# Kernel optimization log

Measured on AMD Instinct MI355X. Metric: run time of the kernel, lower is better.

Reference implementation:

```python
import jax, jax.numpy as jnp
import numpy as np

D_MODEL = 1024
N_HEADS = 16
HEAD_DIM = D_MODEL // N_HEADS  # 64


def setup_inputs() -> dict:
    key = jax.random.key(0)
    k1, k2, k3 = jax.random.split(key, 3)
    B, T = 2, 2048
    x = jax.random.normal(k1, (B, T, D_MODEL), dtype=jnp.float32)
    # nn.Linear(d, 3d) weight applied as x @ W (stored transposed vs torch)
    W_qkv = jax.random.normal(k2, (D_MODEL, 3 * D_MODEL), dtype=jnp.float32) / np.sqrt(D_MODEL)
    W_proj = jax.random.normal(k3, (D_MODEL, D_MODEL), dtype=jnp.float32) / np.sqrt(D_MODEL)
    return {"x": x, "W_qkv": W_qkv, "W_proj": W_proj}


def reference(x, W_qkv, W_proj):
    B, T, D = x.shape
    qkv = x @ W_qkv  # [B, T, 3D]
    qkv = qkv.reshape(B, T, 3, N_HEADS, HEAD_DIM)
    qkv = jnp.transpose(qkv, (2, 0, 3, 1, 4))  # [3, B, H, T, hd]
    q, k, v = qkv[0], qkv[1], qkv[2]
    # muP 'readout' attn_score: scale by 1/head_dim (instead of 1/sqrt(head_dim))
    attn = jnp.einsum('bhqd,bhkd->bhqk', q, k) / HEAD_DIM  # [B, H, T, T]
    attn = jax.nn.softmax(attn, axis=-1)
    out = jnp.einsum('bhqk,bhkd->bhqd', attn, v)  # [B, H, T, hd]
    out = jnp.transpose(out, (0, 2, 1, 3)).reshape(B, T, D)
    return out @ W_proj
```

## Files before the change

### kernel.cpp

```cpp
#include <hip/hip_runtime.h>
#include <hip/hip_bf16.h>
#include <hip/hip_fp16.h>
#include <stdint.h>

#define B_    2
#define T_    2048
#define DM    1024
#define NH    16
#define HD    64
#define M_    (B_ * T_)
#define N_QKV (3 * DM)

typedef __attribute__((ext_vector_type(8))) __bf16 bf16x8;
typedef __attribute__((ext_vector_type(4))) float  v4f;
typedef __attribute__((ext_vector_type(2))) __fp16 fp16x2;
typedef __attribute__((ext_vector_type(4))) _Float16 h4;
typedef __attribute__((ext_vector_type(8))) _Float16 h8;
typedef __hip_bfloat16 bf16;

#define EXP_SC 0.022542110013890053f

__device__ __forceinline__ void gld_lds16(const void* g, void* l) {
  __builtin_amdgcn_global_load_lds(
      (const __attribute__((address_space(1))) void*)(g),
      (__attribute__((address_space(3))) void*)(l), 16, 0, 0);
}


__global__ __launch_bounds__(256) void prep(
    const float* __restrict__ x, const float* __restrict__ Wqkv,
    const float* __restrict__ Wproj, bf16* __restrict__ Xb,
    bf16* __restrict__ WqkvT, bf16* __restrict__ WprojT) {
  const int f = blockIdx.x;
  if (f < 4096) {
    int i = (f * 256 + threadIdx.x) * 4;
    float4 v = *(const float4*)(x + i);
    union { bf16 h[4]; ushort4 u; } r;
    r.h[0] = __float2bfloat16(v.x); r.h[1] = __float2bfloat16(v.y);
    r.h[2] = __float2bfloat16(v.z); r.h[3] = __float2bfloat16(v.w);
    *(ushort4*)(Xb + i) = r.u;
    return;
  }
  __shared__ float tile[32][33];
  const float* in; bf16* out; int C, bx, by;
  if (f < 4096 + 3072) { int g = f - 4096; bx = g % 96; by = g / 96;
                         in = Wqkv;  out = WqkvT;  C = N_QKV; }
  else                 { int g = f - 7168; bx = g % 32; by = g / 32;
                         in = Wproj; out = WprojT; C = DM; }
  const int R = DM;
  int tx = threadIdx.x & 31, ty = threadIdx.x >> 5;
  int c0 = bx * 32, r0 = by * 32;
  #pragma unroll
  for (int i = ty; i < 32; i += 8)
    tile[i][tx] = in[(size_t)(r0 + i) * C + c0 + tx];
  __syncthreads();
  #pragma unroll
  for (int i = ty; i < 32; i += 8)
    out[(size_t)(c0 + i) * R + r0 + tx] = __float2bfloat16(tile[tx][i]);
}

__global__ __launch_bounds__(256) void transpose_v(
    const _Float16* __restrict__ in, _Float16* __restrict__ out) {
  __shared__ _Float16 tl[64][72];
  const int tid = threadIdx.x, bh = blockIdx.y, t0 = blockIdx.x * 64;
  const size_t ib = (size_t)bh * T_ * HD, ob = (size_t)bh * HD * T_;
  #pragma unroll
  for (int i = 0; i < 2; ++i) {
    int flat = (i * 256 + tid) * 8;
    int r = flat >> 6, c = flat & 63;
    *(uint4*)(&tl[r][c]) = *(const uint4*)(in + ib + (size_t)(t0 + r) * HD + c);
  }
  __syncthreads();
  int d = tid >> 2, c0 = (tid & 3) * 16;
  #pragma unroll
  for (int j = 0; j < 16; j += 8) {
    union { _Float16 h[8]; uint4 u; } pk;
    #pragma unroll
    for (int k2 = 0; k2 < 8; ++k2) pk.h[k2] = tl[c0 + j + k2][d];
    *(uint4*)(out + ob + (size_t)d * T_ + t0 + c0 + j) = pk.u;
  }
}

template <int MODE>
__global__ __launch_bounds__(256) void gemm_bt(
    const bf16* __restrict__ A, const bf16* __restrict__ BT,
    float* __restrict__ Cf, bf16* __restrict__ qb, bf16* __restrict__ kb,
    _Float16* __restrict__ vb, int M, int N, int K) {
  __shared__ bf16 As[128 * 64];
  __shared__ bf16 Bs[128 * 64];
  const int tid = threadIdx.x;
  const int l = tid & 63, w = tid >> 6;
  const int wm = w >> 1, wn = w & 1;
  const int m0 = blockIdx.y * 128, n0 = blockIdx.x * 128;
  const int fr = l & 15;
  const int lg = l >> 4;

  v4f acc[4][4] = {};

  for (int kt = 0; kt < K; kt += 64) {
    __syncthreads();
    #pragma unroll
    for (int i = 0; i < 4; ++i) {
      int p = i * 256 + tid;
      int row = p >> 3, g = (p & 7) ^ (row & 7);
      gld_lds16(A + (size_t)(m0 + row) * K + kt + g * 8, As + p * 8);
      gld_lds16(BT + (size_t)(n0 + row) * K + kt + g * 8, Bs + p * 8);
    }
    __syncthreads();
    #pragma unroll
    for (int kk = 0; kk < 64; kk += 32) {
      const int gl = (kk >> 3) + lg;
      bf16x8 af[4], bfr[4];
      #pragma unroll
      for (int i = 0; i < 4; ++i) {
        int row = wm * 64 + i * 16 + fr;
        af[i] = *(const bf16x8*)(As + row * 64 + (gl ^ (fr & 7)) * 8);
      }
      #pragma unroll
      for (int i = 0; i < 4; ++i) {
        int row = wn * 64 + i * 16 + fr;
        bfr[i] = *(const bf16x8*)(Bs + row * 64 + (gl ^ (fr & 7)) * 8);
      }
      #pragma unroll
      for (int mi = 0; mi < 4; ++mi)
        #pragma unroll
        for (int ni = 0; ni < 4; ++ni)
          acc[mi][ni] = __builtin_amdgcn_mfma_f32_16x16x32_bf16(
              af[mi], bfr[ni], acc[mi][ni], 0, 0, 0);
    }
  }

  #pragma unroll
  for (int mi = 0; mi < 4; ++mi) {
    #pragma unroll
    for (int ni = 0; ni < 4; ++ni) {
      #pragma unroll
      for (int r = 0; r < 4; ++r) {
        int gm = m0 + wm * 64 + mi * 16 + (l >> 4) * 4 + r;
        int gn = n0 + wn * 64 + ni * 16 + (l & 15);
        float v = acc[mi][ni][r];
        if constexpr (MODE == 0) {
          Cf[(size_t)gm * N + gn] = v;
        } else {
          int b = gm >> 11, t = gm & 2047;
          int s = gn >> 10, h = (gn >> 6) & 15, d = gn & 63;
          size_t bh = (size_t)(b * NH + h);
          if (s == 0)      qb[(bh * T_ + t) * HD + d] = __float2bfloat16(v * EXP_SC);
          else if (s == 1) kb[(bh * T_ + t) * HD + d] = __float2bfloat16(v);
          else             vb[(bh * T_ + t) * HD + d] = (_Float16)v;
        }
      }
    }
  }
}

__global__ __launch_bounds__(256) void gemm_bt_n64(
    const bf16* __restrict__ A, const bf16* __restrict__ BT,
    float* __restrict__ Cf, int M, int N, int K) {
  __shared__ bf16 As[128 * 64];
  __shared__ bf16 Bs[64 * 64];
  const int tid = threadIdx.x;
  const int l = tid & 63, w = tid >> 6;
  const int wm = w >> 1, wn = w & 1;
  const int m0 = blockIdx.y * 128, n0 = blockIdx.x * 64;
  const int fr = l & 15;
  const int lg = l >> 4;

  v4f acc[4][2] = {};

  for (int kt = 0; kt < K; kt += 64) {
    __syncthreads();
    #pragma unroll
    for (int i = 0; i < 4; ++i) {
      int p = i * 256 + tid;
      int row = p >> 3, g = (p & 7) ^ (row & 7);
      gld_lds16(A + (size_t)(m0 + row) * K + kt + g * 8, As + p * 8);
    }
    #pragma unroll
    for (int i = 0; i < 2; ++i) {
      int p = i * 256 + tid;
      int row = p >> 3, g = (p & 7) ^ (row & 7);
      gld_lds16(BT + (size_t)(n0 + row) * K + kt + g * 8, Bs + p * 8);
    }
    __syncthreads();
    #pragma unroll
    for (int kk = 0; kk < 64; kk += 32) {
      const int gl = (kk >> 3) + lg;
      bf16x8 af[4], bfr[2];
      #pragma unroll
      for (int i = 0; i < 4; ++i) {
        int row = wm * 64 + i * 16 + fr;
        af[i] = *(const bf16x8*)(As + row * 64 + (gl ^ (fr & 7)) * 8);
      }
      #pragma unroll
      for (int i = 0; i < 2; ++i) {
        int row = wn * 32 + i * 16 + fr;
        bfr[i] = *(const bf16x8*)(Bs + row * 64 + (gl ^ (fr & 7)) * 8);
      }
      #pragma unroll
      for (int mi = 0; mi < 4; ++mi)
        #pragma unroll
        for (int ni = 0; ni < 2; ++ni)
          acc[mi][ni] = __builtin_amdgcn_mfma_f32_16x16x32_bf16(
              af[mi], bfr[ni], acc[mi][ni], 0, 0, 0);
    }
  }

  #pragma unroll
  for (int mi = 0; mi < 4; ++mi)
    #pragma unroll
    for (int ni = 0; ni < 2; ++ni)
      #pragma unroll
      for (int r = 0; r < 4; ++r) {
        int gm = m0 + wm * 64 + mi * 16 + (l >> 4) * 4 + r;
        int gn = n0 + wn * 32 + ni * 16 + (l & 15);
        Cf[(size_t)gm * N + gn] = acc[mi][ni][r];
      }
}

__global__ __launch_bounds__(256) void flash_attn(
    const bf16* __restrict__ Qg, const bf16* __restrict__ Kg,
    const _Float16* __restrict__ VTg, bf16* __restrict__ Og) {
  __shared__ char smem[53248];
  bf16*     Ks = (bf16*)smem;
  _Float16* Vs = (_Float16*)(smem + 16384);
  _Float16 (*Ps)[40] = (_Float16(*)[40])(smem + 32768);
  float*    Obuf = (float*)smem;
  float*    Lbuf = (float*)(smem + 34816);

  const int tid = threadIdx.x, l = tid & 63, w = tid >> 6;
  const int qh = w & 1, kh = w >> 1;
  const int fr = l & 15, fk = (l >> 4) * 8, g4 = (l >> 4) * 4, lg = l >> 4;
  const int bh = blockIdx.y, qt = blockIdx.x;
  const int q0 = qt * 128 + qh * 64;
  const size_t base  = (size_t)bh * T_ * HD;
  const size_t baseV = (size_t)bh * HD * T_;
  _Float16 (*Pw)[40] = Ps + w * 64;

  bf16x8 qB[4][2];
  #pragma unroll
  for (int qf = 0; qf < 4; ++qf)
    #pragma unroll
    for (int kki = 0; kki < 2; ++kki)
      qB[qf][kki] = *(const bf16x8*)(
          Qg + base + (size_t)(q0 + qf * 16 + fr) * HD + kki * 32 + fk);

  h8 ones;
  #pragma unroll
  for (int j = 0; j < 8; ++j) ones[j] = (_Float16)1.0f;

  v4f o[4][4] = {};
  v4f lacc[4] = {};

  for (int kt = 0; kt < T_; kt += 128) {
    __syncthreads();
    #pragma unroll
    for (int i = 0; i < 4; ++i) {
      int p = i * 256 + tid;
      int krow = p >> 3, kg = (p & 7) ^ (krow & 7);
      gld_lds16(Kg + base + (size_t)(kt + krow) * HD + kg * 8, Ks + p * 8);
      int vrow = p >> 4, vg = (p & 15) ^ (vrow & 15);
      gld_lds16(VTg + baseV + (size_t)vrow * T_ + kt + vg * 8, Vs + p * 8);
    }
    __syncthreads();

    #pragma unroll
    for (int c = 0; c < 2; ++c) {
      const int kkg = kh * 2 + c;
      #pragma unroll
      for (int hf = 0; hf < 2; ++hf) {
        const int kf = kkg * 2 + hf;
        v4f st[4] = {};
        #pragma unroll
        for (int kki = 0; kki < 2; ++kki) {
          int row = kf * 16 + fr;
          bf16x8 ak = *(const bf16x8*)(
              Ks + row * 64 + ((kki * 4 + lg) ^ (fr & 7)) * 8);
          #pragma unroll
          for (int qf = 0; qf < 4; ++qf)
            st[qf] = __builtin_amdgcn_mfma_f32_16x16x32_bf16(
                ak, qB[qf][kki], st[qf], 0, 0, 0);
        }
        #pragma unroll
        for (int qf = 0; qf < 4; ++qf) {
          union { fp16x2 p2[2]; h4 p4; } u;
          u.p2[0] = __builtin_amdgcn_cvt_pkrtz(
              __builtin_amdgcn_exp2f(st[qf][0]),
              __builtin_amdgcn_exp2f(st[qf][1]));
          u.p2[1] = __builtin_amdgcn_cvt_pkrtz(
              __builtin_amdgcn_exp2f(st[qf][2]),
              __builtin_amdgcn_exp2f(st[qf][3]));
          *(h4*)(&Pw[qf * 16 + fr][hf * 16 + g4]) = u.p4;
        }
      }
      h8 ap[4], bv[4];
      #pragma unroll
      for (int qf = 0; qf < 4; ++qf)
        ap[qf] = *(const h8*)(&Pw[qf * 16 + fr][fk]);
      #pragma unroll
      for (int nf = 0; nf < 4; ++nf) {
        int row = nf * 16 + fr;
        bv[nf] = *(const h8*)(Vs + row * 128 + ((kkg * 4 + lg) ^ fr) * 8);
      }
      #pragma unroll
      for (int qf = 0; qf < 4; ++qf) {
        lacc[qf] = __builtin_amdgcn_mfma_f32_16x16x32_f16(
            ap[qf], ones, lacc[qf], 0, 0, 0);
        #pragma unroll
        for (int nf = 0; nf < 4; ++nf)
          o[qf][nf] = __builtin_amdgcn_mfma_f32_16x16x32_f16(
              ap[qf], bv[nf], o[qf][nf], 0, 0, 0);
      }
    }
  }

  __syncthreads();
  if (w >= 2) {
    #pragma unroll
    for (int qf = 0; qf < 4; ++qf)
      #pragma unroll
      for (int r = 0; r < 4; ++r) {
        int row = qf * 16 + g4 + r;
        #pragma unroll
        for (int nf = 0; nf < 4; ++nf)
          Obuf[(qh * 64 + row) * 68 + nf * 16 + fr] = o[qf][nf][r];
        if (fr == 0) Lbuf[qh * 64 + row] = lacc[qf][r];
      }
  }
  __syncthreads();
  if (w < 2) {
    int b = bh >> 4, h = bh & 15;
    #pragma unroll
    for (int qf = 0; qf < 4; ++qf) {
      #pragma unroll
      for (int r = 0; r < 4; ++r) {
        int row = qf * 16 + g4 + r;
        float inv = 1.f / (lacc[qf][r] + Lbuf[qh * 64 + row]);
        int t = q0 + row;
        #pragma unroll
        for (int nf = 0; nf < 4; ++nf) {
          float val = o[qf][nf][r] + Obuf[(qh * 64 + row) * 68 + nf * 16 + fr];
          Og[((size_t)(b * T_ + t)) * DM + h * HD + nf * 16 + fr] =
              __float2bfloat16(val * inv);
        }
      }
    }
  }
}

extern "C" void kernel_launch(void* const* d_in, const int* in_sizes, int n_in,
                              void* d_out, int out_size, void* d_ws, size_t ws_size,
                              hipStream_t stream) {
  const float* x     = (const float*)d_in[0];
  const float* Wqkv  = (const float*)d_in[1];
  const float* Wproj = (const float*)d_in[2];
  float* out = (float*)d_out;
  char* ws = (char*)d_ws;

  bf16*     Xb     = (bf16*)(ws);
  bf16*     WqkvT  = (bf16*)(ws + (size_t)( 8u << 20));
  bf16*     WprojT = (bf16*)(ws + (size_t)(14u << 20));
  bf16*     Qb     = (bf16*)(ws + (size_t)(16u << 20));
  bf16*     Kb     = (bf16*)(ws + (size_t)(24u << 20));
  _Float16* VTh    = (_Float16*)(ws + (size_t)(32u << 20));
  _Float16* Vh     = (_Float16*)(ws + (size_t)(40u << 20));
  bf16*     Ab     = (bf16*)(ws + (size_t)(40u << 20));

  prep<<<8192, 256, 0, stream>>>(x, Wqkv, Wproj, Xb, WqkvT, WprojT);

  gemm_bt<1><<<dim3(N_QKV / 128, M_ / 128), 256, 0, stream>>>(
      Xb, WqkvT, nullptr, Qb, Kb, Vh, M_, N_QKV, DM);

  transpose_v<<<dim3(T_ / 64, B_ * NH), 256, 0, stream>>>(Vh, VTh);

  flash_attn<<<dim3(T_ / 128, B_ * NH), 256, 0, stream>>>(Qb, Kb, VTh, Ab);

  gemm_bt_n64<<<dim3(DM / 64, M_ / 128), 256, 0, stream>>>(
      Ab, WprojT, out, M_, DM, DM);
}
```

Baseline: 188.4 us.

## Fuse V transpose into QKV GEMM epilogue and split attention keys across blocks

The QKV GEMM now writes V already transposed, staging it through shared memory in its epilogue, so the separate transpose kernel is gone. Flash attention is split into two key halves via grid z to double the block count. Each half atomically adds its unnormalized output and row sums into fp32 buffers, and a new normalize kernel converts them to bf16. This adds two memsets, atomics traffic and an extra pass over a 16MB fp32 buffer in exchange for more parallelism. Summation order of the atomics is nondeterministic.

New measurement: 258.4 us. +37.2%, slower.

```diff
diff --git a/kernel.cpp b/kernel.cpp
--- a/kernel.cpp
+++ b/kernel.cpp
@@ -59,41 +59,21 @@
     out[(size_t)(c0 + i) * R + r0 + tx] = __float2bfloat16(tile[tx][i]);
 }
 
-__global__ __launch_bounds__(256) void transpose_v(
-    const _Float16* __restrict__ in, _Float16* __restrict__ out) {
-  __shared__ _Float16 tl[64][72];
-  const int tid = threadIdx.x, bh = blockIdx.y, t0 = blockIdx.x * 64;
-  const size_t ib = (size_t)bh * T_ * HD, ob = (size_t)bh * HD * T_;
-  #pragma unroll
-  for (int i = 0; i < 2; ++i) {
-    int flat = (i * 256 + tid) * 8;
-    int r = flat >> 6, c = flat & 63;
-    *(uint4*)(&tl[r][c]) = *(const uint4*)(in + ib + (size_t)(t0 + r) * HD + c);
-  }
-  __syncthreads();
-  int d = tid >> 2, c0 = (tid & 3) * 16;
-  #pragma unroll
-  for (int j = 0; j < 16; j += 8) {
-    union { _Float16 h[8]; uint4 u; } pk;
-    #pragma unroll
-    for (int k2 = 0; k2 < 8; ++k2) pk.h[k2] = tl[c0 + j + k2][d];
-    *(uint4*)(out + ob + (size_t)d * T_ + t0 + c0 + j) = pk.u;
-  }
-}
-
 template <int MODE>
 __global__ __launch_bounds__(256) void gemm_bt(
     const bf16* __restrict__ A, const bf16* __restrict__ BT,
     float* __restrict__ Cf, bf16* __restrict__ qb, bf16* __restrict__ kb,
-    _Float16* __restrict__ vb, int M, int N, int K) {
-  __shared__ bf16 As[128 * 64];
-  __shared__ bf16 Bs[128 * 64];
+    _Float16* __restrict__ vtb, int M, int N, int K) {
+  __shared__ char smem[35840];
+  bf16* As = (bf16*)smem;
+  bf16* Bs = (bf16*)(smem + 16384);
   const int tid = threadIdx.x;
   const int l = tid & 63, w = tid >> 6;
   const int wm = w >> 1, wn = w & 1;
   const int m0 = blockIdx.y * 128, n0 = blockIdx.x * 128;
   const int fr = l & 15;
   const int lg = l >> 4;
+  const int g4 = lg * 4;
 
   v4f acc[4][4] = {};
 
@@ -130,14 +110,49 @@
     }
   }
 
+  if constexpr (MODE == 1) {
+    if (n0 >= 2048) {
+      const int b = m0 >> 11;
+      const int vt0 = m0 & 2047;
+      const int hbase = ((n0 - 2048) >> 6) & 15;
+      _Float16 (*Vt)[136] = (_Float16(*)[136])smem;
+      #pragma unroll
+      for (int half = 0; half < 2; ++half) {
+        __syncthreads();
+        if (wn == half) {
+          #pragma unroll
+          for (int mi = 0; mi < 4; ++mi) {
+            int trow = wm * 64 + mi * 16 + g4;
+            #pragma unroll
+            for (int ni = 0; ni < 4; ++ni) {
+              h4 pv;
+              #pragma unroll
+              for (int r = 0; r < 4; ++r) pv[r] = (_Float16)acc[mi][ni][r];
+              *(h4*)(&Vt[ni * 16 + fr][trow]) = pv;
+            }
+          }
+        }
+        __syncthreads();
+        size_t bh = (size_t)(b * NH + ((hbase + half) & 15));
+        #pragma unroll
+        for (int i = 0; i < 4; ++i) {
+          int p = i * 256 + tid;
+          int d = p >> 4, tg = (p & 15) * 8;
+          *(uint4*)(vtb + (bh * HD + d) * T_ + vt0 + tg) = *(uint4*)(&Vt[d][tg]);
+        }
+      }
+      return;
+    }
+  }
+
   #pragma unroll
   for (int mi = 0; mi < 4; ++mi) {
     #pragma unroll
     for (int ni = 0; ni < 4; ++ni) {
       #pragma unroll
       for (int r = 0; r < 4; ++r) {
-        int gm = m0 + wm * 64 + mi * 16 + (l >> 4) * 4 + r;
-        int gn = n0 + wn * 64 + ni * 16 + (l & 15);
+        int gm = m0 + wm * 64 + mi * 16 + g4 + r;
+        int gn = n0 + wn * 64 + ni * 16 + fr;
         float v = acc[mi][ni][r];
         if constexpr (MODE == 0) {
           Cf[(size_t)gm * N + gn] = v;
@@ -145,9 +160,8 @@
           int b = gm >> 11, t = gm & 2047;
           int s = gn >> 10, h = (gn >> 6) & 15, d = gn & 63;
           size_t bh = (size_t)(b * NH + h);
-          if (s == 0)      qb[(bh * T_ + t) * HD + d] = __float2bfloat16(v * EXP_SC);
-          else if (s == 1) kb[(bh * T_ + t) * HD + d] = __float2bfloat16(v);
-          else             vb[(bh * T_ + t) * HD + d] = (_Float16)v;
+          if (s == 0) qb[(bh * T_ + t) * HD + d] = __float2bfloat16(v * EXP_SC);
+          else        kb[(bh * T_ + t) * HD + d] = __float2bfloat16(v);
         }
       }
     }
@@ -220,7 +234,8 @@
 
 __global__ __launch_bounds__(256) void flash_attn(
     const bf16* __restrict__ Qg, const bf16* __restrict__ Kg,
-    const _Float16* __restrict__ VTg, bf16* __restrict__ Og) {
+    const _Float16* __restrict__ VTg, float* __restrict__ Oacc,
+    float* __restrict__ Lacc) {
   __shared__ char smem[53248];
   bf16*     Ks = (bf16*)smem;
   _Float16* Vs = (_Float16*)(smem + 16384);
@@ -232,6 +247,7 @@
   const int qh = w & 1, kh = w >> 1;
   const int fr = l & 15, fk = (l >> 4) * 8, g4 = (l >> 4) * 4, lg = l >> 4;
   const int bh = blockIdx.y, qt = blockIdx.x;
+  const int kz0 = (int)blockIdx.z * 1024;
   const int q0 = qt * 128 + qh * 64;
   const size_t base  = (size_t)bh * T_ * HD;
   const size_t baseV = (size_t)bh * HD * T_;
@@ -252,7 +268,7 @@
   v4f o[4][4] = {};
   v4f lacc[4] = {};
 
-  for (int kt = 0; kt < T_; kt += 128) {
+  for (int kt = kz0; kt < kz0 + 1024; kt += 128) {
     __syncthreads();
     #pragma unroll
     for (int i = 0; i < 4; ++i) {
@@ -335,17 +351,31 @@
       #pragma unroll
       for (int r = 0; r < 4; ++r) {
         int row = qf * 16 + g4 + r;
-        float inv = 1.f / (lacc[qf][r] + Lbuf[qh * 64 + row]);
         int t = q0 + row;
+        float lsum = lacc[qf][r] + Lbuf[qh * 64 + row];
+        if (fr == 0)
+          unsafeAtomicAdd(&Lacc[(((size_t)(b * T_ + t)) << 4) + h], lsum);
         #pragma unroll
         for (int nf = 0; nf < 4; ++nf) {
           float val = o[qf][nf][r] + Obuf[(qh * 64 + row) * 68 + nf * 16 + fr];
-          Og[((size_t)(b * T_ + t)) * DM + h * HD + nf * 16 + fr] =
-              __float2bfloat16(val * inv);
-        }
-      }
-    }
-  }
+          unsafeAtomicAdd(
+              &Oacc[(size_t)(b * T_ + t) * DM + h * HD + nf * 16 + fr], val);
+        }
+      }
+    }
+  }
+}
+
+__global__ __launch_bounds__(256) void normalize(
+    const float* __restrict__ Oacc, const float* __restrict__ Lacc,
+    bf16* __restrict__ Ab) {
+  int i = (blockIdx.x * 256 + threadIdx.x) * 4;
+  float4 v = *(const float4*)(Oacc + i);
+  float inv = 1.0f / Lacc[((size_t)(i >> 10) << 4) + ((i & 1023) >> 6)];
+  union { bf16 h[4]; ushort4 u; } r;
+  r.h[0] = __float2bfloat16(v.x * inv); r.h[1] = __float2bfloat16(v.y * inv);
+  r.h[2] = __float2bfloat16(v.z * inv); r.h[3] = __float2bfloat16(v.w * inv);
+  *(ushort4*)(Ab + i) = r.u;
 }
 
 extern "C" void kernel_launch(void* const* d_in, const int* in_sizes, int n_in,
@@ -359,21 +389,26 @@
 
   bf16*     Xb     = (bf16*)(ws);
   bf16*     WqkvT  = (bf16*)(ws + (size_t)( 8u << 20));
-  bf16*     WprojT = (bf16*)(ws + (size_t)(14u << 20));
+  float*    Oacc   = (float*)(ws);
   bf16*     Qb     = (bf16*)(ws + (size_t)(16u << 20));
+  bf16*     Ab     = (bf16*)(ws + (size_t)(16u << 20));
   bf16*     Kb     = (bf16*)(ws + (size_t)(24u << 20));
   _Float16* VTh    = (_Float16*)(ws + (size_t)(32u << 20));
-  _Float16* Vh     = (_Float16*)(ws + (size_t)(40u << 20));
-  bf16*     Ab     = (bf16*)(ws + (size_t)(40u << 20));
+  bf16*     WprojT = (bf16*)(ws + (size_t)(40u << 20));
+  float*    Lacc   = (float*)(ws + (size_t)(42u << 20));
 
   prep<<<8192, 256, 0, stream>>>(x, Wqkv, Wproj, Xb, WqkvT, WprojT);
 
   gemm_bt<1><<<dim3(N_QKV / 128, M_ / 128), 256, 0, stream>>>(
-      Xb, WqkvT, nullptr, Qb, Kb, Vh, M_, N_QKV, DM);
-
-  transpose_v<<<dim3(T_ / 64, B_ * NH), 256, 0, stream>>>(Vh, VTh);
-
-  flash_attn<<<dim3(T_ / 128, B_ * NH), 256, 0, stream>>>(Qb, Kb, VTh, Ab);
+      Xb, WqkvT, nullptr, Qb, Kb, VTh, M_, N_QKV, DM);
+
+  (void)hipMemsetAsync(Oacc, 0, (size_t)M_ * DM * sizeof(float), stream);
+  (void)hipMemsetAsync(Lacc, 0, (size_t)M_ * NH * sizeof(float), stream);
+
+  flash_attn<<<dim3(T_ / 128, B_ * NH, 2), 256, 0, stream>>>(
+      Qb, Kb, VTh, Oacc, Lacc);
+
+  normalize<<<(M_ * DM) / 1024, 256, 0, stream>>>(Oacc, Lacc, Ab);
 
   gemm_bt_n64<<<dim3(DM / 64, M_ / 128), 256, 0, stream>>>(
       Ab, WprojT, out, M_, DM, DM);
```
